# Kernel tuning notes

Hardware: AMD Instinct MI355X
Metric: run time of the kernel (lower is better)

## Reference

```python
import jax, jax.numpy as jnp
import numpy as np

N_NODES = 50000
N_EDGES = 800000
T = 3          # number of graph snapshots
L = 2          # num_layers
D = 128        # node feat dim == hidden dim
DE = 16        # edge feat dim


def setup_inputs() -> dict:
    key = jax.random.key(0)
    ks = jax.random.split(key, 12)
    return {
        "src": jax.random.randint(ks[0], (T, N_EDGES), 0, N_NODES, dtype=jnp.int32),
        "dst": jax.random.randint(ks[1], (T, N_EDGES), 0, N_NODES, dtype=jnp.int32),
        "n_feats": jax.random.normal(ks[2], (T, N_NODES, D), dtype=jnp.float32),
        "e_feats": jax.random.normal(ks[3], (T, N_EDGES, DE), dtype=jnp.float32),
        "W0": jax.random.normal(ks[4], (L, D, D), dtype=jnp.float32) * (1.0 / np.sqrt(D)),
        "lstm_Wih": jax.random.normal(ks[5], (L, 4 * D, D), dtype=jnp.float32) * (1.0 / np.sqrt(D)),
        "lstm_Whh": jax.random.normal(ks[6], (L, 4 * D, D), dtype=jnp.float32) * (1.0 / np.sqrt(D)),
        "lstm_bih": jnp.zeros((L, 4 * D), dtype=jnp.float32),
        "lstm_bhh": jnp.zeros((L, 4 * D), dtype=jnp.float32),
        "a_w": jax.random.normal(ks[7], (L, 2 * D + DE), dtype=jnp.float32) * 0.05,
    }


def _lstm(x, Wih, Whh, bih, bhh):
    # x: [S, H] unbatched sequence (S = D rows of W). PyTorch gate order i,f,g,o.
    H = Whh.shape[1]
    b = bih + bhh

    def step(carry, xt):
        h, c = carry
        gates = Wih @ xt + Whh @ h + b          # [4H]
        i = jax.nn.sigmoid(gates[:H])
        f = jax.nn.sigmoid(gates[H:2 * H])
        g = jnp.tanh(gates[2 * H:3 * H])
        o = jax.nn.sigmoid(gates[3 * H:])
        c = f * c + i * g
        h = o * jnp.tanh(c)
        return (h, c), h

    init = (jnp.zeros((H,), x.dtype), jnp.zeros((H,), x.dtype))
    _, hs = jax.lax.scan(step, init, x)
    return hs  # [S, H]


def _gat(src, dst, nf, ef, W, a_w, n_nodes):
    D_ = nf.shape[1]
    a_src, a_edge, a_dst = a_w[:D_], a_w[D_:D_ + ef.shape[1]], a_w[D_ + ef.shape[1]:]
    ft = nf @ W                                  # [N, H]
    s_src = nf @ a_src                           # [N]
    s_dst = nf @ a_dst                           # [N]
    score = s_src[src] + ef @ a_edge + s_dst[dst]  # [E]
    # edge softmax over destination neighborhoods
    mx = jax.ops.segment_max(score, dst, num_segments=n_nodes)
    ex = jnp.exp(score - mx[dst])
    den = jax.ops.segment_sum(ex, dst, num_segments=n_nodes)
    den = jnp.where(den == 0, 1.0, den)
    alpha = ex / den[dst]                        # [E]
    out = jax.ops.segment_sum(ft[src] * alpha[:, None], dst, num_segments=n_nodes)
    return jax.nn.leaky_relu(out)                # [N, H]


def reference(src, dst, n_feats, e_feats, W0, lstm_Wih, lstm_Whh, lstm_bih, lstm_bhh, a_w):
    n_nodes = n_feats.shape[1]
    feats = [n_feats[j] for j in range(n_feats.shape[0])]
    for i in range(W0.shape[0]):
        W = W0[i]
        for j in range(len(feats)):
            W = _lstm(W, lstm_Wih[i], lstm_Whh[i], lstm_bih[i], lstm_bhh[i])
            feats[j] = _gat(src[j], dst[j], feats[j], e_feats[j], W, a_w[i], n_nodes)
    return feats[-1]
```

## Files before the change

kernel.cpp:

```cpp
#include <hip/hip_runtime.h>
#include <cstdint>
#include <cstddef>

#define N_NODES 50000
#define N_EDGES 800000
#define D 128
#define DE 16
#define HB 1563
#define NB512 98

typedef float v2f __attribute__((ext_vector_type(2)));


__device__ void lstm_pre_body(const float* __restrict__ Wih,
     const float* __restrict__ bih, const float* __restrict__ bhh,
     const float* __restrict__ xin, float* __restrict__ P, int bid){
  __shared__ float xs[128];
  int i = bid >> 7, t = bid & 127;
  const float* x = xin + (size_t)i*16384;
  if (threadIdx.x < 128) xs[threadIdx.x] = x[t*128 + threadIdx.x];
  __syncthreads();
  int r = threadIdx.x;
  const float4* wr = (const float4*)(Wih + (size_t)(i*512 + r)*128);
  const float4* x4 = (const float4*)xs;
  float acc = bih[i*512+r] + bhh[i*512+r];
  #pragma unroll
  for (int k=0;k<32;k++){
    float4 w = wr[k]; float4 xv = x4[k];
    acc += w.x*xv.x + w.y*xv.y + w.z*xv.z + w.w*xv.w;
  }
  P[(size_t)(i*128+t)*512 + r] = acc;
}

__device__ void lstm_scan_body(const float* __restrict__ Whh,
     const float* __restrict__ P, float* __restrict__ xout, int i){
  __shared__ float hs[128];
  __shared__ float part[4][512];
  const int r  = threadIdx.x;
  const int w  = r >> 6;
  const int l  = r & 63;
  const int kc = w >> 1;
  const int rh = w & 1;
  const int row0 = rh*256 + l*4;
  v2f wv[4][16];
  {
    const float* base = Whh + (size_t)i*512*128 + (size_t)row0*128 + kc*32;
    #pragma unroll
    for (int ri=0; ri<4; ri++){
      const v2f* p2 = (const v2f*)(base + ri*128);
      #pragma unroll
      for (int j=0;j<16;j++) wv[ri][j] = p2[j];
    }
  }
  float c = 0.f;
  float hreg = 0.f;
  if (r < 128) hs[r] = 0.f;
  __syncthreads();
  const float* Pi = P + (size_t)i*128*512;
  float* xo = xout + (size_t)i*128*128;
  for (int t=0; t<128; t++){
    float p0=0.f, p1=0.f, p2=0.f, p3=0.f;
    if (r < 128){
      p0 = Pi[t*512 +   0 + r];
      p1 = Pi[t*512 + 128 + r];
      p2 = Pi[t*512 + 256 + r];
      p3 = Pi[t*512 + 384 + r];
    }
    float4 hbuf[8];
    {
      const float4* h4 = ((const float4*)hs) + kc*8;
      #pragma unroll
      for (int j=0;j<8;j++) hbuf[j] = h4[j];
    }
    const v2f* h2 = (const v2f*)hbuf;
    v2f a0 = (v2f)(0.f), a1 = (v2f)(0.f), a2 = (v2f)(0.f), a3 = (v2f)(0.f);
    #pragma unroll
    for (int j=0;j<16;j++){
      v2f hv = h2[j];
      a0 = __builtin_elementwise_fma(wv[0][j], hv, a0);
      a1 = __builtin_elementwise_fma(wv[1][j], hv, a1);
      a2 = __builtin_elementwise_fma(wv[2][j], hv, a2);
      a3 = __builtin_elementwise_fma(wv[3][j], hv, a3);
    }
    float4 pr;
    pr.x = a0.x + a0.y;
    pr.y = a1.x + a1.y;
    pr.z = a2.x + a2.y;
    pr.w = a3.x + a3.y;
    *(float4*)&part[kc][row0] = pr;
    __syncthreads();
    if (r < 128){
      int j = r;
      float s0 = ((part[0][      j] + part[1][      j]) + (part[2][      j] + part[3][      j])) + p0;
      float s1 = ((part[0][128 + j] + part[1][128 + j]) + (part[2][128 + j] + part[3][128 + j])) + p1;
      float s2 = ((part[0][256 + j] + part[1][256 + j]) + (part[2][256 + j] + part[3][256 + j])) + p2;
      float s3 = ((part[0][384 + j] + part[1][384 + j]) + (part[2][384 + j] + part[3][384 + j])) + p3;
      float gi = __builtin_amdgcn_rcpf(1.f + __expf(-s0));
      float gf = __builtin_amdgcn_rcpf(1.f + __expf(-s1));
      float xg = fminf(fmaxf(s2, -15.f), 15.f);
      float eg = __expf(2.f*xg);
      float gg = (eg - 1.f) * __builtin_amdgcn_rcpf(eg + 1.f);
      float go = __builtin_amdgcn_rcpf(1.f + __expf(-s3));
      c = gf*c + gi*gg;
      float xc = fminf(fmaxf(c, -15.f), 15.f);
      float e2 = __expf(2.f*xc);
      float th = (e2 - 1.f) * __builtin_amdgcn_rcpf(e2 + 1.f);
      hreg = go*th;
      hs[j] = hreg;
    }
    __syncthreads();
    if (r < 128) xo[t*128 + r] = hreg;
  }
}

__device__ void csr_blocksum512(const int* __restrict__ count,
                                int* __restrict__ bsum, int b){
  __shared__ int red[8];
  int t = threadIdx.x;
  int i = b*512 + t;
  int v = (i < N_NODES) ? count[i] : 0;
  #pragma unroll
  for (int off=32; off; off>>=1) v += __shfl_down(v, off);
  if ((t & 63) == 0) red[t>>6] = v;
  __syncthreads();
  if (t == 0){
    int s = 0;
    #pragma unroll
    for (int k=0;k<8;k++) s += red[k];
    bsum[b] = s;
  }
}

__device__ void csr_scan_bsum512(const int* __restrict__ bsum,
                                 int* __restrict__ boff){
  __shared__ int s[512];
  int t = threadIdx.x;
  int v = (t < NB512) ? bsum[t] : 0;
  s[t] = v; __syncthreads();
  for (int off=1; off<512; off<<=1){
    int u = (t >= off) ? s[t-off] : 0;
    __syncthreads(); s[t] += u; __syncthreads();
  }
  if (t < NB512) boff[t] = s[t] - v;
}

__device__ void csr_downsweep512(const int* __restrict__ count,
    const int* __restrict__ boff, int* __restrict__ row_start,
    int* __restrict__ cursor, int b){
  __shared__ int s[512];
  int t = threadIdx.x;
  int i = b*512 + t;
  int v = (i < N_NODES) ? count[i] : 0;
  s[t] = v; __syncthreads();
  for (int off=1; off<512; off<<=1){
    int u = (t >= off) ? s[t-off] : 0;
    __syncthreads(); s[t] += u; __syncthreads();
  }
  int excl = boff[b] + s[t] - v;
  if (i <= N_NODES) row_start[i] = excl;
  if (i <  N_NODES) cursor[i]   = excl;
}

__global__ __launch_bounds__(512) void k_pre(const float* __restrict__ Wih,
     const float* __restrict__ bih, const float* __restrict__ bhh,
     const float* __restrict__ xin, float* __restrict__ P){
  lstm_pre_body(Wih, bih, bhh, xin, P, blockIdx.x);
}

__global__ __launch_bounds__(512, 2) void k_scan_hist_epart(
    const float* __restrict__ Whh, const float* __restrict__ P,
    float* __restrict__ xout, const int* __restrict__ dst,
    int* __restrict__ count, const float* __restrict__ ef,
    const float* __restrict__ aw, float* __restrict__ epart){
  int b = blockIdx.x;
  if (b < 2){ lstm_scan_body(Whh, P, xout, b); return; }
  b -= 2;
  if (b < HB){
    int e = b*512 + threadIdx.x;
    if (e < N_EDGES) atomicAdd(&count[dst[e]], 1);
    return;
  }
  b -= HB;
  int e = b*512 + threadIdx.x;
  if (e < N_EDGES){
    const float4* ev = (const float4*)(ef + (size_t)e*16);
    float4 v0=ev[0], v1=ev[1], v2=ev[2], v3=ev[3];
    #pragma unroll
    for (int l=0; l<2; l++){
      const float4* A = (const float4*)(aw + l*272 + 128);
      float4 A0=A[0], A1=A[1], A2=A[2], A3=A[3];
      float acc = v0.x*A0.x + v0.y*A0.y + v0.z*A0.z + v0.w*A0.w;
      acc      += v1.x*A1.x + v1.y*A1.y + v1.z*A1.z + v1.w*A1.w;
      acc      += v2.x*A2.x + v2.y*A2.y + v2.z*A2.z + v2.w*A2.w;
      acc      += v3.x*A3.x + v3.y*A3.y + v3.z*A3.z + v3.w*A3.w;
      epart[(size_t)l*N_EDGES + e] = acc;
    }
  }
}

__global__ __launch_bounds__(512) void k_pre_blocksum(const float* __restrict__ Wih,
     const float* __restrict__ bih, const float* __restrict__ bhh,
     const float* __restrict__ xin, float* __restrict__ P,
     const int* __restrict__ count, int* __restrict__ bsum){
  if (blockIdx.x < 256) lstm_pre_body(Wih, bih, bhh, xin, P, blockIdx.x);
  else                  csr_blocksum512(count, bsum, blockIdx.x - 256);
}

__global__ __launch_bounds__(512, 2) void k_scan_scanbsum(
    const float* __restrict__ Whh, const float* __restrict__ P,
    float* __restrict__ xout, const int* __restrict__ bsum,
    int* __restrict__ boff){
  if (blockIdx.x < 2) lstm_scan_body(Whh, P, xout, blockIdx.x);
  else                csr_scan_bsum512(bsum, boff);
}

__global__ __launch_bounds__(512) void k_pre_downsweep(const float* __restrict__ Wih,
     const float* __restrict__ bih, const float* __restrict__ bhh,
     const float* __restrict__ xin, float* __restrict__ P,
     const int* __restrict__ count, const int* __restrict__ boff,
     int* __restrict__ row_start, int* __restrict__ cursor){
  if (blockIdx.x < 256) lstm_pre_body(Wih, bih, bhh, xin, P, blockIdx.x);
  else                  csr_downsweep512(count, boff, row_start, cursor, blockIdx.x - 256);
}

__global__ __launch_bounds__(512, 2) void k_scan_scatter(
    const float* __restrict__ Whh, const float* __restrict__ P,
    float* __restrict__ xout, const int* __restrict__ src,
    const int* __restrict__ dst, int* __restrict__ cursor,
    int* __restrict__ perm, int* __restrict__ src_perm){
  int b = blockIdx.x;
  if (b < 2){ lstm_scan_body(Whh, P, xout, b); return; }
  int e = (b-2)*512 + threadIdx.x;
  if (e >= N_EDGES) return;
  int d = dst[e];
  int pos = atomicAdd(&cursor[d], 1);
  perm[pos] = e;
  src_perm[pos] = src[e];
}

__global__ __launch_bounds__(256) void gat_transform(const float* __restrict__ f,
    const float* __restrict__ W, const float* __restrict__ aw,
    float* __restrict__ ft, float* __restrict__ s_src){
  __shared__ float Ws[64*128];
  __shared__ float fs[128*36];
  int n0 = blockIdx.x * 32;
  {
    int n = threadIdx.x >> 3, kq = threadIdx.x & 7;
    int gn = n0 + n;
    #pragma unroll
    for (int p=0;p<4;p++){
      int k = kq*16 + p*4;
      float4 v = make_float4(0.f,0.f,0.f,0.f);
      if (gn < N_NODES) v = *(const float4*)(f + (size_t)gn*128 + k);
      fs[(k+0)*36+n] = v.x; fs[(k+1)*36+n] = v.y;
      fs[(k+2)*36+n] = v.z; fs[(k+3)*36+n] = v.w;
    }
  }
  int jg = threadIdx.x & 31, ng = threadIdx.x >> 5;
  v2f A00=(v2f)(0.f), A01=A00, A10=A00, A11=A00;
  v2f A20=A00, A21=A00, A30=A00, A31=A00;
  for (int kk=0; kk<128; kk+=64){
    __syncthreads();
    {
      const float4* W4 = (const float4*)(W + (size_t)kk*128);
      float4* Ws4w = (float4*)Ws;
      for (int idx = threadIdx.x; idx < 2048; idx += 256) Ws4w[idx] = W4[idx];
    }
    __syncthreads();
    const float4* Ws4 = (const float4*)Ws;
    #pragma unroll 4
    for (int k2=0;k2<64;k2++){
      float4 wvv = Ws4[k2*32 + jg];
      v2f wl; wl.x = wvv.x; wl.y = wvv.y;
      v2f wh; wh.x = wvv.z; wh.y = wvv.w;
      float4 fv = *(const float4*)&fs[(kk+k2)*36 + (ng<<2)];
      v2f f0 = (v2f)(fv.x), f1 = (v2f)(fv.y), f2 = (v2f)(fv.z), f3 = (v2f)(fv.w);
      A00 = __builtin_elementwise_fma(wl, f0, A00);
      A01 = __builtin_elementwise_fma(wh, f0, A01);
      A10 = __builtin_elementwise_fma(wl, f1, A10);
      A11 = __builtin_elementwise_fma(wh, f1, A11);
      A20 = __builtin_elementwise_fma(wl, f2, A20);
      A21 = __builtin_elementwise_fma(wh, f2, A21);
      A30 = __builtin_elementwise_fma(wl, f3, A30);
      A31 = __builtin_elementwise_fma(wh, f3, A31);
    }
  }
  int nb = n0 + (ng<<2);
  float4 o0; o0.x=A00.x; o0.y=A00.y; o0.z=A01.x; o0.w=A01.y;
  float4 o1; o1.x=A10.x; o1.y=A10.y; o1.z=A11.x; o1.w=A11.y;
  float4 o2; o2.x=A20.x; o2.y=A20.y; o2.z=A21.x; o2.w=A21.y;
  float4 o3; o3.x=A30.x; o3.y=A30.y; o3.z=A31.x; o3.w=A31.y;
  if (nb+0 < N_NODES) *(float4*)(ft + (size_t)(nb+0)*128 + (jg<<2)) = o0;
  if (nb+1 < N_NODES) *(float4*)(ft + (size_t)(nb+1)*128 + (jg<<2)) = o1;
  if (nb+2 < N_NODES) *(float4*)(ft + (size_t)(nb+2)*128 + (jg<<2)) = o2;
  if (nb+3 < N_NODES) *(float4*)(ft + (size_t)(nb+3)*128 + (jg<<2)) = o3;
  if (threadIdx.x < 32){
    int gn = n0 + threadIdx.x;
    if (gn < N_NODES){
      float s = 0.f;
      for (int k=0;k<128;k++) s += fs[k*36 + threadIdx.x] * aw[k];
      s_src[gn] = s;
    }
  }
}

__global__ __launch_bounds__(256) void gat_edge_score(const int* __restrict__ perm,
    const int* __restrict__ src_perm, const float* __restrict__ s_src,
    const float* __restrict__ epart_l, float* __restrict__ score){
  int p = blockIdx.x*256 + threadIdx.x;
  if (p >= N_EDGES) return;
  score[p] = s_src[src_perm[p]] + epart_l[perm[p]];
}

__global__ __launch_bounds__(256) void gat_aggregate(const int* __restrict__ row_start,
    const int* __restrict__ src_perm, float* __restrict__ score,
    const float* __restrict__ ft, float* __restrict__ out){
  int lane = threadIdx.x & 63;
  int wv = threadIdx.x >> 6;
  int n = blockIdx.x*4 + wv;
  if (n >= N_NODES) return;
  int s = row_start[n], e = row_start[n+1];
  float m = -1e30f;
  for (int p = s+lane; p < e; p += 64) m = fmaxf(m, score[p]);
  #pragma unroll
  for (int off=32; off; off>>=1) m = fmaxf(m, __shfl_xor(m, off));
  float den = 0.f;
  for (int p = s+lane; p < e; p += 64){
    float ex = __expf(score[p]-m);
    den += ex;
    score[p] = ex;
  }
  #pragma unroll
  for (int off=32; off; off>>=1) den += __shfl_xor(den, off);
  float inv = (den > 0.f) ? 1.f/den : 0.f;
  float a0 = 0.f, a1 = 0.f;
  for (int p = s; p < e; p++){
    float al = score[p]*inv;
    int sp = src_perm[p];
    float2 v = ((const float2*)(ft + (size_t)sp*128))[lane];
    a0 += al*v.x; a1 += al*v.y;
  }
  float2 o;
  o.x = (a0 > 0.f) ? a0 : 0.01f*a0;
  o.y = (a1 > 0.f) ? a1 : 0.01f*a1;
  ((float2*)(out + (size_t)n*128))[lane] = o;
}

extern "C" void kernel_launch(void* const* d_in, const int* in_sizes, int n_in,
                              void* d_out, int out_size, void* d_ws, size_t ws_size,
                              hipStream_t stream){
  (void)in_sizes; (void)n_in; (void)out_size; (void)ws_size;
  const int*   src     = (const int*)d_in[0] + (size_t)2*N_EDGES;
  const int*   dst     = (const int*)d_in[1] + (size_t)2*N_EDGES;
  const float* n_feats = (const float*)d_in[2] + (size_t)2*N_NODES*D;
  const float* e_feats = (const float*)d_in[3] + (size_t)2*N_EDGES*DE;
  const float* W0      = (const float*)d_in[4];
  const float* Wih     = (const float*)d_in[5];
  const float* Whh     = (const float*)d_in[6];
  const float* bih     = (const float*)d_in[7];
  const float* bhh     = (const float*)d_in[8];
  const float* a_w     = (const float*)d_in[9];
  float* out = (float*)d_out;

  char* wsp = (char*)d_ws;
  auto alloc = [&](size_t bytes)->char*{
    char* p = wsp; wsp += (bytes + 255) & ~(size_t)255; return p;
  };
  float* P         = (float*)alloc((size_t)2*128*512*4);
  float* xA        = (float*)alloc((size_t)2*128*128*4);
  float* xB        = (float*)alloc((size_t)2*128*128*4);
  int*   count     = (int*)  alloc((size_t)N_NODES*4);
  int*   bsum      = (int*)  alloc((size_t)NB512*4);
  int*   boff      = (int*)  alloc((size_t)NB512*4);
  int*   row_start = (int*)  alloc((size_t)(N_NODES+1)*4);
  int*   cursor    = (int*)  alloc((size_t)N_NODES*4);
  int*   perm      = (int*)  alloc((size_t)N_EDGES*4);
  int*   src_perm  = (int*)  alloc((size_t)N_EDGES*4);
  float* score     = (float*)alloc((size_t)N_EDGES*4);
  float* s_src     = (float*)alloc((size_t)N_NODES*4);
  float* epart     = (float*)alloc((size_t)2*N_EDGES*4);
  float* ft        = (float*)alloc((size_t)N_NODES*D*4);
  float* f1        = (float*)alloc((size_t)N_NODES*D*4);

  hipMemsetAsync(count, 0, (size_t)N_NODES*4, stream);

  k_pre            <<<256,        512, 0, stream>>>(Wih, bih, bhh, W0, P);
  k_scan_hist_epart<<<2 + 2*HB,   512, 0, stream>>>(Whh, P, xA, dst, count,
                                                    e_feats, a_w, epart);
  k_pre_blocksum   <<<256 + NB512,512, 0, stream>>>(Wih, bih, bhh, xA, P,
                                                    count, bsum);
  k_scan_scanbsum  <<<3,          512, 0, stream>>>(Whh, P, xB, bsum, boff);
  k_pre_downsweep  <<<256 + NB512,512, 0, stream>>>(Wih, bih, bhh, xB, P,
                                                    count, boff, row_start, cursor);
  k_scan_scatter   <<<2 + HB,     512, 0, stream>>>(Whh, P, xA, src, dst,
                                                    cursor, perm, src_perm);
  const float* Wfin = xA;

  const float* fin = n_feats;
  for (int l=0; l<2; l++){
    float* outl = (l==0) ? f1 : out;
    gat_transform <<<(N_NODES+31)/32, 256, 0, stream>>>(fin, Wfin + (size_t)l*16384,
                                                        a_w + (size_t)l*272, ft, s_src);
    gat_edge_score<<<(N_EDGES+255)/256, 256, 0, stream>>>(perm, src_perm, s_src,
                                                          epart + (size_t)l*N_EDGES, score);
    gat_aggregate <<<N_NODES/4, 256, 0, stream>>>(row_start, src_perm, score, ft, outl);
    fin = f1;
  }
}
```

Measured before the change: 838.3 us.

## Fuse edge scoring into aggregate with online softmax and packed edge records

Removes the separate gat_edge_score kernel. The scatter step now writes a packed int4 record per sorted edge holding the source index and both layers' edge-feature scores. gat_aggregate computes each edge score from s_src plus the packed value and uses an online max/sum softmax, which folds two passes over the edges into one. The exp is recomputed in the weighted-sum loop. This saves one launch per layer and the indirect perm gathers, at the cost of 16-byte edge records and extra exp work.

```diff
diff --git a/kernel.cpp b/kernel.cpp
--- a/kernel.cpp
+++ b/kernel.cpp
@@ -171,7 +171,7 @@
     const float* __restrict__ Whh, const float* __restrict__ P,
     float* __restrict__ xout, const int* __restrict__ dst,
     int* __restrict__ count, const float* __restrict__ ef,
-    const float* __restrict__ aw, float* __restrict__ epart){
+    const float* __restrict__ aw, float2* __restrict__ epart){
   int b = blockIdx.x;
   if (b < 2){ lstm_scan_body(Whh, P, xout, b); return; }
   b -= 2;
@@ -185,16 +185,26 @@
   if (e < N_EDGES){
     const float4* ev = (const float4*)(ef + (size_t)e*16);
     float4 v0=ev[0], v1=ev[1], v2=ev[2], v3=ev[3];
-    #pragma unroll
-    for (int l=0; l<2; l++){
-      const float4* A = (const float4*)(aw + l*272 + 128);
+    float2 r;
+    {
+      const float4* A = (const float4*)(aw + 128);
       float4 A0=A[0], A1=A[1], A2=A[2], A3=A[3];
       float acc = v0.x*A0.x + v0.y*A0.y + v0.z*A0.z + v0.w*A0.w;
       acc      += v1.x*A1.x + v1.y*A1.y + v1.z*A1.z + v1.w*A1.w;
       acc      += v2.x*A2.x + v2.y*A2.y + v2.z*A2.z + v2.w*A2.w;
       acc      += v3.x*A3.x + v3.y*A3.y + v3.z*A3.z + v3.w*A3.w;
-      epart[(size_t)l*N_EDGES + e] = acc;
-    }
+      r.x = acc;
+    }
+    {
+      const float4* A = (const float4*)(aw + 272 + 128);
+      float4 A0=A[0], A1=A[1], A2=A[2], A3=A[3];
+      float acc = v0.x*A0.x + v0.y*A0.y + v0.z*A0.z + v0.w*A0.w;
+      acc      += v1.x*A1.x + v1.y*A1.y + v1.z*A1.z + v1.w*A1.w;
+      acc      += v2.x*A2.x + v2.y*A2.y + v2.z*A2.z + v2.w*A2.w;
+      acc      += v3.x*A3.x + v3.y*A3.y + v3.z*A3.z + v3.w*A3.w;
+      r.y = acc;
+    }
+    epart[e] = r;
   }
 }
 
@@ -226,16 +236,21 @@
 __global__ __launch_bounds__(512, 2) void k_scan_scatter(
     const float* __restrict__ Whh, const float* __restrict__ P,
     float* __restrict__ xout, const int* __restrict__ src,
-    const int* __restrict__ dst, int* __restrict__ cursor,
-    int* __restrict__ perm, int* __restrict__ src_perm){
+    const int* __restrict__ dst, const float2* __restrict__ epart,
+    int* __restrict__ cursor, int4* __restrict__ edat){
   int b = blockIdx.x;
   if (b < 2){ lstm_scan_body(Whh, P, xout, b); return; }
   int e = (b-2)*512 + threadIdx.x;
   if (e >= N_EDGES) return;
   int d = dst[e];
+  float2 ep = epart[e];
   int pos = atomicAdd(&cursor[d], 1);
-  perm[pos] = e;
-  src_perm[pos] = src[e];
+  int4 v;
+  v.x = src[e];
+  v.y = __float_as_int(ep.x);
+  v.z = __float_as_int(ep.y);
+  v.w = 0;
+  edat[pos] = v;
 }
 
 __global__ __launch_bounds__(256) void gat_transform(const float* __restrict__ f,
@@ -304,39 +319,39 @@
   }
 }
 
-__global__ __launch_bounds__(256) void gat_edge_score(const int* __restrict__ perm,
-    const int* __restrict__ src_perm, const float* __restrict__ s_src,
-    const float* __restrict__ epart_l, float* __restrict__ score){
-  int p = blockIdx.x*256 + threadIdx.x;
-  if (p >= N_EDGES) return;
-  score[p] = s_src[src_perm[p]] + epart_l[perm[p]];
-}
-
 __global__ __launch_bounds__(256) void gat_aggregate(const int* __restrict__ row_start,
-    const int* __restrict__ src_perm, float* __restrict__ score,
-    const float* __restrict__ ft, float* __restrict__ out){
+    const int4* __restrict__ edat, const float* __restrict__ s_src,
+    float* __restrict__ score, const float* __restrict__ ft,
+    float* __restrict__ out, int layer){
   int lane = threadIdx.x & 63;
   int wv = threadIdx.x >> 6;
   int n = blockIdx.x*4 + wv;
   if (n >= N_NODES) return;
   int s = row_start[n], e = row_start[n+1];
   float m = -1e30f;
-  for (int p = s+lane; p < e; p += 64) m = fmaxf(m, score[p]);
-  #pragma unroll
-  for (int off=32; off; off>>=1) m = fmaxf(m, __shfl_xor(m, off));
   float den = 0.f;
   for (int p = s+lane; p < e; p += 64){
-    float ex = __expf(score[p]-m);
-    den += ex;
-    score[p] = ex;
+    int4 v = edat[p];
+    float el = __int_as_float(layer ? v.z : v.y);
+    float sc = s_src[v.x] + el;
+    score[p] = sc;
+    float nm = fmaxf(m, sc);
+    den = den*__expf(m - nm) + __expf(sc - nm);
+    m = nm;
   }
   #pragma unroll
-  for (int off=32; off; off>>=1) den += __shfl_xor(den, off);
+  for (int off=32; off; off>>=1){
+    float m2 = __shfl_xor(m, off);
+    float d2 = __shfl_xor(den, off);
+    float nm = fmaxf(m, m2);
+    den = den*__expf(m - nm) + d2*__expf(m2 - nm);
+    m = nm;
+  }
   float inv = (den > 0.f) ? 1.f/den : 0.f;
   float a0 = 0.f, a1 = 0.f;
   for (int p = s; p < e; p++){
-    float al = score[p]*inv;
-    int sp = src_perm[p];
+    float al = __expf(score[p] - m)*inv;
+    int sp = edat[p].x;
     float2 v = ((const float2*)(ft + (size_t)sp*128))[lane];
     a0 += al*v.x; a1 += al*v.y;
   }
@@ -366,21 +381,20 @@
   auto alloc = [&](size_t bytes)->char*{
     char* p = wsp; wsp += (bytes + 255) & ~(size_t)255; return p;
   };
-  float* P         = (float*)alloc((size_t)2*128*512*4);
-  float* xA        = (float*)alloc((size_t)2*128*128*4);
-  float* xB        = (float*)alloc((size_t)2*128*128*4);
-  int*   count     = (int*)  alloc((size_t)N_NODES*4);
-  int*   bsum      = (int*)  alloc((size_t)NB512*4);
-  int*   boff      = (int*)  alloc((size_t)NB512*4);
-  int*   row_start = (int*)  alloc((size_t)(N_NODES+1)*4);
-  int*   cursor    = (int*)  alloc((size_t)N_NODES*4);
-  int*   perm      = (int*)  alloc((size_t)N_EDGES*4);
-  int*   src_perm  = (int*)  alloc((size_t)N_EDGES*4);
-  float* score     = (float*)alloc((size_t)N_EDGES*4);
-  float* s_src     = (float*)alloc((size_t)N_NODES*4);
-  float* epart     = (float*)alloc((size_t)2*N_EDGES*4);
-  float* ft        = (float*)alloc((size_t)N_NODES*D*4);
-  float* f1        = (float*)alloc((size_t)N_NODES*D*4);
+  float*  P         = (float*) alloc((size_t)2*128*512*4);
+  float*  xA        = (float*) alloc((size_t)2*128*128*4);
+  float*  xB        = (float*) alloc((size_t)2*128*128*4);
+  int*    count     = (int*)   alloc((size_t)N_NODES*4);
+  int*    bsum      = (int*)   alloc((size_t)NB512*4);
+  int*    boff      = (int*)   alloc((size_t)NB512*4);
+  int*    row_start = (int*)   alloc((size_t)(N_NODES+1)*4);
+  int*    cursor    = (int*)   alloc((size_t)N_NODES*4);
+  int4*   edat      = (int4*)  alloc((size_t)N_EDGES*16);
+  float*  score     = (float*) alloc((size_t)N_EDGES*4);
+  float2* epart     = (float2*)alloc((size_t)N_EDGES*8);
+  float*  s_src     = (float*) alloc((size_t)N_NODES*4);
+  float*  ft        = (float*) alloc((size_t)N_NODES*D*4);
+  float*  f1        = (float*) alloc((size_t)N_NODES*D*4);
 
   hipMemsetAsync(count, 0, (size_t)N_NODES*4, stream);
 
@@ -393,17 +407,16 @@
   k_pre_downsweep  <<<256 + NB512,512, 0, stream>>>(Wih, bih, bhh, xB, P,
                                                     count, boff, row_start, cursor);
   k_scan_scatter   <<<2 + HB,     512, 0, stream>>>(Whh, P, xA, src, dst,
-                                                    cursor, perm, src_perm);
+                                                    epart, cursor, edat);
   const float* Wfin = xA;
 
   const float* fin = n_feats;
   for (int l=0; l<2; l++){
     float* outl = (l==0) ? f1 : out;
-    gat_transform <<<(N_NODES+31)/32, 256, 0, stream>>>(fin, Wfin + (size_t)l*16384,
-                                                        a_w + (size_t)l*272, ft, s_src);
-    gat_edge_score<<<(N_EDGES+255)/256, 256, 0, stream>>>(perm, src_perm, s_src,
-                                                          epart + (size_t)l*N_EDGES, score);
-    gat_aggregate <<<N_NODES/4, 256, 0, stream>>>(row_start, src_perm, score, ft, outl);
+    gat_transform<<<(N_NODES+31)/32, 256, 0, stream>>>(fin, Wfin + (size_t)l*16384,
+                                                       a_w + (size_t)l*272, ft, s_src);
+    gat_aggregate<<<N_NODES/4, 256, 0, stream>>>(row_start, edat, s_src,
+                                                 score, ft, outl, l);
     fin = f1;
   }
 }
```

Result: no change. 826.8 us (-1.4%).
